# Performance work log

Measured on AMD Instinct MI355X. Metric: run time of the kernel, lower is better.

The kernel has to match this reference:

```python
import jax, jax.numpy as jnp
import numpy as np

T, B, S, D = 512, 32, 512, 512
EPS = 1e-6  # LayerNorm eps


def _ln(x, g, b):
    m = jnp.mean(x, axis=-1, keepdims=True)
    v = jnp.mean((x - m) ** 2, axis=-1, keepdims=True)
    return g * (x - m) * jax.lax.rsqrt(v + EPS) + b


def setup_inputs() -> dict:
    key = jax.random.key(0)
    ks = jax.random.split(key, 10)
    sc = 1.0 / np.sqrt(D).astype(np.float32)
    return {
        "prev_layer": jax.random.normal(ks[0], (T, B, D), jnp.float32),
        "hidden": jax.random.normal(ks[1], (B, D), jnp.float32),
        "enc_output": jax.random.normal(ks[2], (B, S, D), jnp.float32),
        "memory_length": jax.random.randint(ks[3], (B,), 1, S + 1),
        # nn.Linear weights stored as [in, out] (transposed torch layout)
        "W_in": jax.random.normal(ks[4], (D, 3 * D), jnp.float32) * sc,
        "W_enc": jax.random.normal(ks[5], (D, D), jnp.float32) * sc,
        "W_attn_in": jax.random.normal(ks[6], (D, D), jnp.float32) * sc,
        "W_hidden": jax.random.normal(ks[7], (D, D), jnp.float32) * sc,
        "W_ctx": jax.random.normal(ks[8], (D, D), jnp.float32) * sc,
        # LayerNorm gains/biases (5 LNs)
        "g_pre": jnp.ones((3 * D,), jnp.float32), "b_pre": jnp.zeros((3 * D,), jnp.float32),
        "g_enc": jnp.ones((D,), jnp.float32), "b_enc": jnp.zeros((D,), jnp.float32),
        "g_attn": jnp.ones((D,), jnp.float32), "b_attn": jnp.zeros((D,), jnp.float32),
        "g_h": jnp.ones((D,), jnp.float32), "b_h": jnp.zeros((D,), jnp.float32),
        "g_c": jnp.ones((D,), jnp.float32), "b_c": jnp.zeros((D,), jnp.float32),
    }


def reference(prev_layer, hidden, enc_output, W_in, W_enc, W_attn_in, W_hidden,
              W_ctx, g_pre, b_pre, g_enc, b_enc, g_attn, b_attn, g_h, b_h,
              g_c, b_c, memory_length):
    d = prev_layer.shape[-1]
    sqrt_d = jnp.sqrt(jnp.asarray(d, prev_layer.dtype))
    # dropout is identity in eval mode
    preact = _ln(prev_layer @ W_in, g_pre, b_pre)          # [T,B,3D]
    pctx = _ln(enc_output @ W_enc, g_enc, b_enc)           # [B,S,D]
    z, h_gate, pl_t = jnp.split(preact, 3, axis=-1)
    z = jax.nn.sigmoid(z)
    h_gate = jax.nn.sigmoid(h_gate)

    # SRU-style linear recurrence: s_t = (1-z_t)*s_{t-1} + z_t*pl_t
    def step(h, zp):
        z_t, p_t = zp
        s = (1.0 - z_t) * h + z_t * p_t
        return s, s

    hidden_last, ss = jax.lax.scan(step, hidden, (z, pl_t))  # ss: [T,B,D]

    attn_in = _ln(ss @ W_attn_in, g_attn, b_attn)            # [T,B,D]
    align = jnp.einsum('tbd,bsd->bts', attn_in, pctx)        # [B,T,S]
    mask = jnp.arange(pctx.shape[1])[None, :] < memory_length[:, None]  # [B,S]
    align = jnp.where(mask[:, None, :], align, -jnp.inf)
    av = jax.nn.softmax(align / sqrt_d, axis=-1)             # [B,T,S]
    c = jnp.einsum('bts,bsd->tbd', av, pctx)                 # [T,B,D]
    attn_out = c / sqrt_d

    trans = _ln(ss @ W_hidden, g_h, b_h) + _ln(attn_out @ W_ctx, g_c, b_c)
    out = jnp.tanh(trans)
    out = (1.0 - h_gate) * out + h_gate * prev_layer         # [T,B,D]
    p_attn = jnp.transpose(av, (1, 0, 2))                    # [T,B,S]
    return out, hidden_last, p_attn
```

## Files before the change

### kernel.cpp

```cpp
#include <hip/hip_runtime.h>
#include <hip/hip_bf16.h>
#include <cmath>

#define T_ 512
#define B_ 32
#define S_ 512
#define D_ 512
#define D3_ 1536
#define NCH 16
#define CT (T_ / NCH)
static constexpr float LN_EPS = 1e-6f;
static constexpr float RSQRT_D = 0.044194173824159216f;

typedef __attribute__((ext_vector_type(8))) __bf16 bf16x8;
typedef __attribute__((ext_vector_type(4))) float f32x4;

struct __align__(4) bfx2 { __hip_bfloat16 x, y; };
struct __align__(8) bfx4 { __hip_bfloat16 x, y, z, w; };

__device__ __forceinline__ void g2l16(const void* g, void* l) {
    __builtin_amdgcn_global_load_lds(
        (const __attribute__((address_space(1))) unsigned int*)g,
        (__attribute__((address_space(3))) unsigned int*)l, 16, 0, 0);
}

__device__ __forceinline__ float blk_sum(float v, float* sm) {
    v += __shfl_down(v, 32); v += __shfl_down(v, 16); v += __shfl_down(v, 8);
    v += __shfl_down(v, 4);  v += __shfl_down(v, 2);  v += __shfl_down(v, 1);
    int w = threadIdx.x >> 6;
    if ((threadIdx.x & 63) == 0) sm[w] = v;
    __syncthreads();
    float r = sm[0] + sm[1] + sm[2] + sm[3];
    __syncthreads();
    return r;
}

__device__ __forceinline__ float blk_max(float v, float* sm) {
    v = fmaxf(v, __shfl_down(v, 32)); v = fmaxf(v, __shfl_down(v, 16));
    v = fmaxf(v, __shfl_down(v, 8));  v = fmaxf(v, __shfl_down(v, 4));
    v = fmaxf(v, __shfl_down(v, 2));  v = fmaxf(v, __shfl_down(v, 1));
    int w = threadIdx.x >> 6;
    if ((threadIdx.x & 63) == 0) sm[w] = v;
    __syncthreads();
    float r = fmaxf(fmaxf(sm[0], sm[1]), fmaxf(sm[2], sm[3]));
    __syncthreads();
    return r;
}

template <typename OT>
__global__ __launch_bounds__(256) void gemm_bt(
    const __hip_bfloat16* __restrict__ A, int lda, long Abs,
    const __hip_bfloat16* __restrict__ B, int ldb, long Bbs,
    OT* __restrict__ C, long ldc, long Cbs,
    int K, float alpha)
{
    __shared__ __align__(16) __hip_bfloat16 As[128 * 32];
    __shared__ __align__(16) __hip_bfloat16 Bs[128 * 32];

    const int bz = blockIdx.z;
    A += (long)bz * Abs; B += (long)bz * Bbs; C += (long)bz * Cbs;
    const long bm = (long)blockIdx.y * 128, bn = (long)blockIdx.x * 128;

    const int tid = threadIdx.x, lane = tid & 63, w = tid >> 6;
    const int wm = (w >> 1) * 64, wn = (w & 1) * 64;
    const int srow = lane >> 2;
    const int skB = (lane & 3) * 16;

    f32x4 acc[4][4];
#pragma unroll
    for (int i = 0; i < 4; i++)
#pragma unroll
        for (int j = 0; j < 4; j++) acc[i][j] = (f32x4)(0.0f);

    const char* ga0 = (const char*)(A + (bm + w * 16 + srow) * (long)lda) + skB;
    const char* ga1 = (const char*)(A + (bm + (w + 4) * 16 + srow) * (long)lda) + skB;
    const char* gb0 = (const char*)(B + (bn + w * 16 + srow) * (long)ldb) + skB;
    const char* gb1 = (const char*)(B + (bn + (w + 4) * 16 + srow) * (long)ldb) + skB;
    char* la0 = (char*)As + w * 1024 + lane * 16;
    char* la1 = (char*)As + (w + 4) * 1024 + lane * 16;
    char* lb0 = (char*)Bs + w * 1024 + lane * 16;
    char* lb1 = (char*)Bs + (w + 4) * 1024 + lane * 16;

    const char* Ar = (const char*)As + (wm + (lane & 15)) * 64 + (lane >> 4) * 16;
    const char* Br = (const char*)Bs + (wn + (lane & 15)) * 64 + (lane >> 4) * 16;

    for (int k0 = 0; k0 < K; k0 += 32) {
        const long kb = (long)k0 * 2;
        g2l16(ga0 + kb, la0);
        g2l16(ga1 + kb, la1);
        g2l16(gb0 + kb, lb0);
        g2l16(gb1 + kb, lb1);
        __syncthreads();

        bf16x8 af[4], bfr[4];
#pragma unroll
        for (int i = 0; i < 4; i++) {
            af[i] = *(const bf16x8*)(Ar + i * 1024);
            bfr[i] = *(const bf16x8*)(Br + i * 1024);
        }
#pragma unroll
        for (int i = 0; i < 4; i++)
#pragma unroll
            for (int j = 0; j < 4; j++)
                acc[i][j] = __builtin_amdgcn_mfma_f32_16x16x32_bf16(
                    af[i], bfr[j], acc[i][j], 0, 0, 0);
        __syncthreads();
    }

#pragma unroll
    for (int i = 0; i < 4; i++) {
        const long row0 = bm + wm + i * 16 + (lane >> 4) * 4;
#pragma unroll
        for (int j = 0; j < 4; j++) {
            const long col = bn + wn + j * 16 + (lane & 15);
#pragma unroll
            for (int r = 0; r < 4; r++)
                C[(row0 + r) * ldc + col] = (OT)(alpha * acc[i][j][r]);
        }
    }
}

__global__ __launch_bounds__(256) void cvt4(
    const float* __restrict__ x, __hip_bfloat16* __restrict__ y, int n4)
{
    int i = blockIdx.x * 256 + threadIdx.x;
    if (i >= n4) return;
    float4 v = ((const float4*)x)[i];
    bfx4 o;
    o.x = __float2bfloat16(v.x); o.y = __float2bfloat16(v.y);
    o.z = __float2bfloat16(v.z); o.w = __float2bfloat16(v.w);
    ((bfx4*)y)[i] = o;
}

__global__ __launch_bounds__(256) void wtrans(
    const float* __restrict__ w0, const float* __restrict__ w1,
    const float* __restrict__ w2, const float* __restrict__ w3,
    const float* __restrict__ w4, __hip_bfloat16* __restrict__ WT)
{
    int z = blockIdx.z;
    const float* W; long off; int N;
    if (z == 0)      { W = w0; off = 0;                N = 1536; }
    else if (z == 1) { W = w1; off = 786432;           N = 512; }
    else if (z == 2) { W = w2; off = 786432 + 262144;  N = 512; }
    else if (z == 3) { W = w3; off = 786432 + 524288;  N = 512; }
    else             { W = w4; off = 786432 + 786432;  N = 512; }
    int n0 = blockIdx.x * 32, k0 = blockIdx.y * 32;
    if (n0 >= N) return;
    __shared__ float t[32][33];
    int tx = threadIdx.x & 31, ty = threadIdx.x >> 5;
#pragma unroll
    for (int i = 0; i < 4; i++)
        t[ty + i * 8][tx] = W[(long)(k0 + ty + i * 8) * N + n0 + tx];
    __syncthreads();
    __hip_bfloat16* O = WT + off;
#pragma unroll
    for (int i = 0; i < 4; i++)
        O[(long)(n0 + ty + i * 8) * 512 + k0 + tx] =
            __float2bfloat16(t[tx][ty + i * 8]);
}

__global__ __launch_bounds__(256) void ptrans(
    const __hip_bfloat16* __restrict__ src, __hip_bfloat16* __restrict__ dst)
{
    long boff = (long)blockIdx.z * (S_ * D_);
    int d0 = blockIdx.x * 32, s0 = blockIdx.y * 32;
    __shared__ __hip_bfloat16 t[32][34];
    int tx = threadIdx.x & 31, ty = threadIdx.x >> 5;
#pragma unroll
    for (int i = 0; i < 4; i++)
        t[ty + i * 8][tx] = src[boff + (long)(s0 + ty + i * 8) * D_ + d0 + tx];
    __syncthreads();
#pragma unroll
    for (int i = 0; i < 4; i++)
        dst[boff + (long)(d0 + ty + i * 8) * S_ + s0 + tx] = t[tx][ty + i * 8];
}

__global__ __launch_bounds__(256) void ln_rows(
    float* X, const float* __restrict__ g,
    const float* __restrict__ bb, int ncols, int sig_upto)
{
    __shared__ float sm[4];
    float* x = X + (long)blockIdx.x * ncols;
    float s = 0.f, q = 0.f;
    for (int c = threadIdx.x; c < ncols; c += 256) {
        float v = x[c]; s += v; q += v * v;
    }
    s = blk_sum(s, sm);
    q = blk_sum(q, sm);
    float m = s / ncols;
    float rs = rsqrtf(q / ncols - m * m + LN_EPS);
    for (int c = threadIdx.x; c < ncols; c += 256) {
        float v = (x[c] - m) * rs * g[c] + bb[c];
        if (c < sig_upto) v = 1.f / (1.f + __expf(-v));
        x[c] = v;
    }
}

__global__ __launch_bounds__(256) void ln_bf16(
    const float* __restrict__ X, const float* __restrict__ g,
    const float* __restrict__ bb, __hip_bfloat16* __restrict__ Y)
{
    __shared__ float sm[4];
    const float* x = X + (long)blockIdx.x * 512;
    int c = threadIdx.x * 2;
    float2 v = *(const float2*)(x + c);
    float s = v.x + v.y, q = v.x * v.x + v.y * v.y;
    s = blk_sum(s, sm);
    q = blk_sum(q, sm);
    float m = s * (1.f / 512);
    float rs = rsqrtf(q * (1.f / 512) - m * m + LN_EPS);
    float2 gg = *(const float2*)(g + c);
    float2 bv = *(const float2*)(bb + c);
    bfx2 o;
    o.x = __float2bfloat16((v.x - m) * rs * gg.x + bv.x);
    o.y = __float2bfloat16((v.y - m) * rs * gg.y + bv.y);
    *(bfx2*)(Y + (long)blockIdx.x * 512 + c) = o;
}

__global__ __launch_bounds__(256) void scan_part1(
    const float* __restrict__ pre, float* __restrict__ Ap, float* __restrict__ Bp)
{
    int idx = blockIdx.x * 256 + threadIdx.x;
    int c = blockIdx.y;
    const float* pz = pre + (long)(idx >> 9) * D3_ + (idx & 511);
    float A = 1.f, s = 0.f;
    for (int t = c * CT; t < (c + 1) * CT; t++) {
        const float* p = pz + (long)t * (B_ * D3_);
        float z = p[0], pl = p[2 * D_];
        float a = 1.f - z;
        A *= a;
        s = a * s + z * pl;
    }
    Ap[c * 16384 + idx] = A;
    Bp[c * 16384 + idx] = s;
}

__global__ __launch_bounds__(256) void scan_part2(
    const float* __restrict__ Ap, const float* __restrict__ Bp,
    const float* __restrict__ h0, float* __restrict__ sin_,
    float* __restrict__ hlast)
{
    int idx = blockIdx.x * 256 + threadIdx.x;
    float s = h0[idx];
    for (int c = 0; c < NCH; c++) {
        sin_[c * 16384 + idx] = s;
        s = Ap[c * 16384 + idx] * s + Bp[c * 16384 + idx];
    }
    hlast[idx] = s;
}

__global__ __launch_bounds__(256) void scan_part3(
    const float* __restrict__ pre, const float* __restrict__ sin_,
    __hip_bfloat16* __restrict__ ssb)
{
    int idx = blockIdx.x * 256 + threadIdx.x;
    int c = blockIdx.y;
    float s = sin_[c * 16384 + idx];
    const float* pz = pre + (long)(idx >> 9) * D3_ + (idx & 511);
    for (int t = c * CT; t < (c + 1) * CT; t++) {
        const float* p = pz + (long)t * (B_ * D3_);
        float z = p[0], pl = p[2 * D_];
        s += z * (pl - s);
        ssb[(long)t * 16384 + idx] = __float2bfloat16(s);
    }
}

__global__ __launch_bounds__(256) void softmax_mask(
    const float* __restrict__ align, const int* __restrict__ mlen,
    float* __restrict__ pattn, __hip_bfloat16* __restrict__ pattnb)
{
    __shared__ float sm[4];
    int b = blockIdx.x >> 9;
    int t = blockIdx.x & 511;
    const float* arow = align + ((long)b * T_ + t) * S_;
    long orow = ((long)t * B_ + b) * S_;
    int len = mlen[b];

    float mx = -INFINITY;
#pragma unroll
    for (int i = 0; i < 2; i++) {
        int s = threadIdx.x + i * 256;
        float v = (s < len) ? arow[s] : -INFINITY;
        mx = fmaxf(mx, v);
    }
    mx = blk_max(mx, sm);

    float e[2];
    float sum = 0.f;
#pragma unroll
    for (int i = 0; i < 2; i++) {
        int s = threadIdx.x + i * 256;
        float v = (s < len) ? __expf(arow[s] - mx) : 0.f;
        e[i] = v; sum += v;
    }
    sum = blk_sum(sum, sm);
    float inv = 1.f / sum;
#pragma unroll
    for (int i = 0; i < 2; i++) {
        int s = threadIdx.x + i * 256;
        float v = e[i] * inv;
        pattn[orow + s] = v;
        pattnb[orow + s] = __float2bfloat16(v);
    }
}

__global__ __launch_bounds__(256) void final_fuse(
    const float* __restrict__ h1, const float* __restrict__ h2,
    const float* __restrict__ pre, const float* __restrict__ prev,
    const float* __restrict__ g_h, const float* __restrict__ b_h,
    const float* __restrict__ g_c, const float* __restrict__ b_c,
    float* __restrict__ out)
{
    __shared__ float sm[4];
    long row = blockIdx.x;
    const float* x1 = h1 + row * D_;
    const float* x2 = h2 + row * D_;
    float v1[2], v2[2];
    float s1 = 0, q1 = 0, s2 = 0, q2 = 0;
#pragma unroll
    for (int i = 0; i < 2; i++) {
        int c = threadIdx.x + i * 256;
        float a = x1[c], b = x2[c];
        v1[i] = a; v2[i] = b;
        s1 += a; q1 += a * a; s2 += b; q2 += b * b;
    }
    s1 = blk_sum(s1, sm); q1 = blk_sum(q1, sm);
    s2 = blk_sum(s2, sm); q2 = blk_sum(q2, sm);
    float m1 = s1 / D_, m2 = s2 / D_;
    float rs1 = rsqrtf(q1 / D_ - m1 * m1 + LN_EPS);
    float rs2 = rsqrtf(q2 / D_ - m2 * m2 + LN_EPS);
#pragma unroll
    for (int i = 0; i < 2; i++) {
        int c = threadIdx.x + i * 256;
        float t1 = (v1[i] - m1) * rs1 * g_h[c] + b_h[c];
        float t2 = (v2[i] - m2) * rs2 * g_c[c] + b_c[c];
        float o = tanhf(t1 + t2);
        float hg = pre[row * D3_ + D_ + c];
        float pv = prev[row * D_ + c];
        out[row * D_ + c] = (1.f - hg) * o + hg * pv;
    }
}

extern "C" void kernel_launch(void* const* d_in, const int* in_sizes, int n_in,
                              void* d_out, int out_size, void* d_ws, size_t ws_size,
                              hipStream_t stream) {
    const float* prev  = (const float*)d_in[0];
    const float* hid0  = (const float*)d_in[1];
    const float* enc   = (const float*)d_in[2];
    const int*   mlen  = (const int*)  d_in[3];
    const float* W_in  = (const float*)d_in[4];
    const float* W_enc = (const float*)d_in[5];
    const float* W_att = (const float*)d_in[6];
    const float* W_hid = (const float*)d_in[7];
    const float* W_ctx = (const float*)d_in[8];
    const float* g_pre = (const float*)d_in[9];
    const float* b_pre = (const float*)d_in[10];
    const float* g_enc = (const float*)d_in[11];
    const float* b_enc = (const float*)d_in[12];
    const float* g_att = (const float*)d_in[13];
    const float* b_att = (const float*)d_in[14];
    const float* g_h   = (const float*)d_in[15];
    const float* b_h   = (const float*)d_in[16];
    const float* g_c   = (const float*)d_in[17];
    const float* b_c   = (const float*)d_in[18];

    float* out   = (float*)d_out;
    float* hlast = out + (long)T_ * B_ * D_;
    float* pattn = hlast + (long)B_ * D_;

    float* ws = (float*)d_ws;
    const long MBf = 262144;
    float* pre              = ws;
    __hip_bfloat16* WT      = (__hip_bfloat16*)(ws + 96 * MBf);
    __hip_bfloat16* prevb   = (__hip_bfloat16*)(ws + 100 * MBf);
    __hip_bfloat16* encb    = (__hip_bfloat16*)(ws + 116 * MBf);
    float* pctxf            = ws + 132 * MBf;
    __hip_bfloat16* pctxb   = (__hip_bfloat16*)(ws + 164 * MBf);
    __hip_bfloat16* pctxT   = (__hip_bfloat16*)(ws + 180 * MBf);
    __hip_bfloat16* ssb     = (__hip_bfloat16*)(ws + 196 * MBf);
    float* scanA            = ws + 212 * MBf;
    float* scanB            = ws + 213 * MBf;
    float* sinb             = ws + 214 * MBf;
    float* attninf          = ws + 100 * MBf;
    __hip_bfloat16* attninb = (__hip_bfloat16*)(ws + 132 * MBf);
    float* algn             = ws + 212 * MBf;
    __hip_bfloat16* pattnb  = (__hip_bfloat16*)(ws + 148 * MBf);
    __hip_bfloat16* attnoutb= (__hip_bfloat16*)(ws + 100 * MBf);
    float* h1f              = ws + 116 * MBf;
    float* h2f              = ws + 148 * MBf;

    const long R = (long)T_ * B_;
    const __hip_bfloat16* W_inT  = WT;
    const __hip_bfloat16* W_encT = WT + 786432;
    const __hip_bfloat16* W_attT = WT + 786432 + 262144;
    const __hip_bfloat16* W_hidT = WT + 786432 + 524288;
    const __hip_bfloat16* W_ctxT = WT + 786432 + 786432;

    dim3 blk(256);

    cvt4<<<8192, blk, 0, stream>>>(prev, prevb, (int)(R * D_ / 4));
    cvt4<<<8192, blk, 0, stream>>>(enc, encb, (int)(R * D_ / 4));
    wtrans<<<dim3(48, 16, 5), blk, 0, stream>>>(W_in, W_enc, W_att, W_hid, W_ctx,
                                                (__hip_bfloat16*)WT);

    gemm_bt<float><<<dim3(12, 128, 1), blk, 0, stream>>>(
        prevb, D_, 0, W_inT, D_, 0, pre, D3_, 0, D_, 1.f);
    ln_rows<<<R, blk, 0, stream>>>(pre, g_pre, b_pre, D3_, 2 * D_);

    gemm_bt<float><<<dim3(4, 128, 1), blk, 0, stream>>>(
        encb, D_, 0, W_encT, D_, 0, pctxf, D_, 0, D_, 1.f);
    ln_bf16<<<R, blk, 0, stream>>>(pctxf, g_enc, b_enc, pctxb);
    ptrans<<<dim3(16, 16, 32), blk, 0, stream>>>(pctxb, pctxT);

    scan_part1<<<dim3(64, NCH), blk, 0, stream>>>(pre, scanA, scanB);
    scan_part2<<<64, blk, 0, stream>>>(scanA, scanB, hid0, sinb, hlast);
    scan_part3<<<dim3(64, NCH), blk, 0, stream>>>(pre, sinb, ssb);

    gemm_bt<float><<<dim3(4, 128, 1), blk, 0, stream>>>(
        ssb, D_, 0, W_attT, D_, 0, attninf, D_, 0, D_, 1.f);
    ln_bf16<<<R, blk, 0, stream>>>(attninf, g_att, b_att, attninb);

    gemm_bt<float><<<dim3(4, 4, 32), blk, 0, stream>>>(
        attninb, B_ * D_, D_, pctxb, D_, (long)S_ * D_,
        algn, S_, (long)T_ * S_, D_, RSQRT_D);

    softmax_mask<<<B_ * T_, blk, 0, stream>>>(algn, mlen, pattn, pattnb);

    gemm_bt<__hip_bfloat16><<<dim3(4, 4, 32), blk, 0, stream>>>(
        pattnb, B_ * S_, S_, pctxT, S_, (long)D_ * S_,
        attnoutb, B_ * D_, D_, S_, RSQRT_D);

    gemm_bt<float><<<dim3(4, 128, 1), blk, 0, stream>>>(
        ssb, D_, 0, W_hidT, D_, 0, h1f, D_, 0, D_, 1.f);
    gemm_bt<float><<<dim3(4, 128, 1), blk, 0, stream>>>(
        attnoutb, D_, 0, W_ctxT, D_, 0, h2f, D_, 0, D_, 1.f);

    final_fuse<<<R, blk, 0, stream>>>(h1f, h2f, pre, prev,
                                      g_h, b_h, g_c, b_c, out);
}
```

Before: 504.8 us.

## Fuse LayerNorm, softmax and gating epilogues into full-row GEMM kernels

Replaces the generic GEMM plus separate LayerNorm, softmax and final-gating kernels with specialized GEMMs. Each block computes full 512-wide rows so row statistics, the masked softmax and the tanh/gate epilogue can be applied in registers. The input projection now writes bf16 output plus per-row partial sums, and the pre-activation LayerNorm is applied on the fly inside the scan and final kernels. This removes several fp32 intermediate round trips through HBM and many launches. In exchange the new kernels use more registers and shared memory, and 64-row tiles give fewer blocks (256 per GEMM), which may lower occupancy.

After: 574.0 us. +13.7%, slower.

```diff
diff --git a/kernel.cpp b/kernel.cpp
--- a/kernel.cpp
+++ b/kernel.cpp
@@ -15,7 +15,6 @@
 typedef __attribute__((ext_vector_type(8))) __bf16 bf16x8;
 typedef __attribute__((ext_vector_type(4))) float f32x4;
 
-struct __align__(4) bfx2 { __hip_bfloat16 x, y; };
 struct __align__(8) bfx4 { __hip_bfloat16 x, y, z, w; };
 
 __device__ __forceinline__ void g2l16(const void* g, void* l) {
@@ -24,47 +23,34 @@
         (__attribute__((address_space(3))) unsigned int*)l, 16, 0, 0);
 }
 
-__device__ __forceinline__ float blk_sum(float v, float* sm) {
-    v += __shfl_down(v, 32); v += __shfl_down(v, 16); v += __shfl_down(v, 8);
-    v += __shfl_down(v, 4);  v += __shfl_down(v, 2);  v += __shfl_down(v, 1);
-    int w = threadIdx.x >> 6;
-    if ((threadIdx.x & 63) == 0) sm[w] = v;
-    __syncthreads();
-    float r = sm[0] + sm[1] + sm[2] + sm[3];
-    __syncthreads();
-    return r;
-}
-
-__device__ __forceinline__ float blk_max(float v, float* sm) {
-    v = fmaxf(v, __shfl_down(v, 32)); v = fmaxf(v, __shfl_down(v, 16));
-    v = fmaxf(v, __shfl_down(v, 8));  v = fmaxf(v, __shfl_down(v, 4));
-    v = fmaxf(v, __shfl_down(v, 2));  v = fmaxf(v, __shfl_down(v, 1));
-    int w = threadIdx.x >> 6;
-    if ((threadIdx.x & 63) == 0) sm[w] = v;
-    __syncthreads();
-    float r = fmaxf(fmaxf(sm[0], sm[1]), fmaxf(sm[2], sm[3]));
-    __syncthreads();
-    return r;
-}
-
-template <typename OT>
-__global__ __launch_bounds__(256) void gemm_bt(
-    const __hip_bfloat16* __restrict__ A, int lda, long Abs,
-    const __hip_bfloat16* __restrict__ B, int ldb, long Bbs,
-    OT* __restrict__ C, long ldc, long Cbs,
-    int K, float alpha)
-{
-    __shared__ __align__(16) __hip_bfloat16 As[128 * 32];
-    __shared__ __align__(16) __hip_bfloat16 Bs[128 * 32];
-
-    const int bz = blockIdx.z;
-    A += (long)bz * Abs; B += (long)bz * Bbs; C += (long)bz * Cbs;
-    const long bm = (long)blockIdx.y * 128, bn = (long)blockIdx.x * 128;
-
+__device__ __forceinline__ float xr_sum16(float v) {
+    v += __shfl_xor(v, 1); v += __shfl_xor(v, 2);
+    v += __shfl_xor(v, 4); v += __shfl_xor(v, 8); return v;
+}
+__device__ __forceinline__ float xr_max16(float v) {
+    v = fmaxf(v, __shfl_xor(v, 1)); v = fmaxf(v, __shfl_xor(v, 2));
+    v = fmaxf(v, __shfl_xor(v, 4)); v = fmaxf(v, __shfl_xor(v, 8)); return v;
+}
+
+__device__ __forceinline__ float sigmoidf_(float x) {
+    return 1.f / (1.f + __expf(-x));
+}
+
+__global__ __launch_bounds__(256) void gemm_pre(
+    const __hip_bfloat16* __restrict__ A,
+    const __hip_bfloat16* __restrict__ Bw,
+    __hip_bfloat16* __restrict__ preb,
+    float2* __restrict__ part)
+{
+    __shared__ char smem[16384];
+    __hip_bfloat16* As = (__hip_bfloat16*)smem;
+    __hip_bfloat16* Bs = (__hip_bfloat16*)(smem + 8192);
+
+    const int m0 = blockIdx.y * 128, n0 = blockIdx.x * 128;
     const int tid = threadIdx.x, lane = tid & 63, w = tid >> 6;
     const int wm = (w >> 1) * 64, wn = (w & 1) * 64;
-    const int srow = lane >> 2;
-    const int skB = (lane & 3) * 16;
+    const int srow = lane >> 2, skB = (lane & 3) * 16;
+    const int q = lane >> 4, c = lane & 15;
 
     f32x4 acc[4][4];
 #pragma unroll
@@ -72,26 +58,24 @@
 #pragma unroll
         for (int j = 0; j < 4; j++) acc[i][j] = (f32x4)(0.0f);
 
-    const char* ga0 = (const char*)(A + (bm + w * 16 + srow) * (long)lda) + skB;
-    const char* ga1 = (const char*)(A + (bm + (w + 4) * 16 + srow) * (long)lda) + skB;
-    const char* gb0 = (const char*)(B + (bn + w * 16 + srow) * (long)ldb) + skB;
-    const char* gb1 = (const char*)(B + (bn + (w + 4) * 16 + srow) * (long)ldb) + skB;
+    const char* ga0 = (const char*)(A + (long)(m0 + w * 16 + srow) * 512) + skB;
+    const char* ga1 = (const char*)(A + (long)(m0 + (w + 4) * 16 + srow) * 512) + skB;
+    const char* gb0 = (const char*)(Bw + (long)(n0 + w * 16 + srow) * 512) + skB;
+    const char* gb1 = (const char*)(Bw + (long)(n0 + (w + 4) * 16 + srow) * 512) + skB;
     char* la0 = (char*)As + w * 1024 + lane * 16;
     char* la1 = (char*)As + (w + 4) * 1024 + lane * 16;
     char* lb0 = (char*)Bs + w * 1024 + lane * 16;
     char* lb1 = (char*)Bs + (w + 4) * 1024 + lane * 16;
-
-    const char* Ar = (const char*)As + (wm + (lane & 15)) * 64 + (lane >> 4) * 16;
-    const char* Br = (const char*)Bs + (wn + (lane & 15)) * 64 + (lane >> 4) * 16;
-
-    for (int k0 = 0; k0 < K; k0 += 32) {
+    const char* Ar = (const char*)As + (wm + c) * 64 + q * 16;
+    const char* Br = (const char*)Bs + (wn + c) * 64 + q * 16;
+
+    for (int k0 = 0; k0 < 512; k0 += 32) {
         const long kb = (long)k0 * 2;
         g2l16(ga0 + kb, la0);
         g2l16(ga1 + kb, la1);
         g2l16(gb0 + kb, lb0);
         g2l16(gb1 + kb, lb1);
         __syncthreads();
-
         bf16x8 af[4], bfr[4];
 #pragma unroll
         for (int i = 0; i < 4; i++) {
@@ -107,15 +91,374 @@
         __syncthreads();
     }
 
-#pragma unroll
-    for (int i = 0; i < 4; i++) {
-        const long row0 = bm + wm + i * 16 + (lane >> 4) * 4;
-#pragma unroll
-        for (int j = 0; j < 4; j++) {
-            const long col = bn + wn + j * 16 + (lane & 15);
-#pragma unroll
-            for (int r = 0; r < 4; r++)
-                C[(row0 + r) * ldc + col] = (OT)(alpha * acc[i][j][r]);
+    float2* sred = (float2*)smem;
+#pragma unroll
+    for (int i = 0; i < 4; i++)
+#pragma unroll
+        for (int r = 0; r < 4; r++) {
+            float s = 0.f, qq = 0.f;
+#pragma unroll
+            for (int j = 0; j < 4; j++) {
+                float v = acc[i][j][r]; s += v; qq += v * v;
+            }
+            s = xr_sum16(s); qq = xr_sum16(qq);
+            if (c == 0) sred[(wm + i * 16 + q * 4 + r) * 2 + (w & 1)] =
+                make_float2(s, qq);
+        }
+    __syncthreads();
+    if ((w & 1) == 0 && c == 0) {
+#pragma unroll
+        for (int i = 0; i < 4; i++)
+#pragma unroll
+            for (int r = 0; r < 4; r++) {
+                int row = wm + i * 16 + q * 4 + r;
+                float2 a = sred[row * 2], b2 = sred[row * 2 + 1];
+                part[(long)blockIdx.x * 16384 + m0 + row] =
+                    make_float2(a.x + b2.x, a.y + b2.y);
+            }
+    }
+    __syncthreads();
+
+    for (int p = 0; p < 2; p++) {
+        if ((w >> 1) == p) {
+#pragma unroll
+            for (int i = 0; i < 4; i++)
+#pragma unroll
+                for (int j = 0; j < 4; j++)
+#pragma unroll
+                    for (int r = 0; r < 4; r++) {
+                        int row = i * 16 + q * 4 + r;
+                        int col = wn + j * 16 + c;
+                        ((__hip_bfloat16*)smem)[row * 128 + col] =
+                            __float2bfloat16(acc[i][j][r]);
+                    }
+        }
+        __syncthreads();
+#pragma unroll
+        for (int rnd = 0; rnd < 4; rnd++) {
+            int row = rnd * 16 + (tid >> 4);
+            int ch = tid & 15;
+            uint4 v = *(const uint4*)(smem + row * 256 + ch * 16);
+            long grow = m0 + p * 64 + row;
+            *(uint4*)((char*)preb + grow * 3072 + (long)n0 * 2 + ch * 16) = v;
+        }
+        __syncthreads();
+    }
+}
+
+__device__ __forceinline__ void rows_core(
+    const __hip_bfloat16* A, long lda,
+    const __hip_bfloat16* B, long ldb, int K,
+    char* smem, f32x4 (&acc)[4][8])
+{
+    const int tid = threadIdx.x, lane = tid & 63, w = tid >> 6;
+#pragma unroll
+    for (int m = 0; m < 4; m++)
+#pragma unroll
+        for (int j = 0; j < 8; j++) acc[m][j] = (f32x4)(0.0f);
+
+    const char* ga = (const char*)(A + (long)(w * 16 + (lane >> 2)) * lda) + (lane & 3) * 16;
+    char* la = smem + w * 1024 + lane * 16;
+    const char* gb = (const char*)(B + (long)(w * 128 + (lane >> 2)) * ldb) + (lane & 3) * 16;
+    char* lb = smem + 4096 + w * 8192 + lane * 16;
+    const long ldbB16 = (long)ldb * 32;
+    const char* Ar = smem + (lane & 15) * 64 + (lane >> 4) * 16;
+    const char* Br = smem + 4096 + (w * 128 + (lane & 15)) * 64 + (lane >> 4) * 16;
+
+    for (int k0 = 0; k0 < K; k0 += 32) {
+        const long kb = (long)k0 * 2;
+        g2l16(ga + kb, la);
+#pragma unroll
+        for (int s = 0; s < 8; s++) g2l16(gb + kb + s * ldbB16, lb + s * 1024);
+        __syncthreads();
+        bf16x8 af[4], bfr[8];
+#pragma unroll
+        for (int m = 0; m < 4; m++) af[m] = *(const bf16x8*)(Ar + m * 1024);
+#pragma unroll
+        for (int j = 0; j < 8; j++) bfr[j] = *(const bf16x8*)(Br + j * 1024);
+#pragma unroll
+        for (int m = 0; m < 4; m++)
+#pragma unroll
+            for (int j = 0; j < 8; j++)
+                acc[m][j] = __builtin_amdgcn_mfma_f32_16x16x32_bf16(
+                    af[m], bfr[j], acc[m][j], 0, 0, 0);
+        __syncthreads();
+    }
+}
+
+__global__ __launch_bounds__(256, 2) void gemm_ln(
+    const __hip_bfloat16* __restrict__ A, long lda,
+    const __hip_bfloat16* __restrict__ W,
+    const float* __restrict__ g, const float* __restrict__ bb,
+    __hip_bfloat16* __restrict__ out)
+{
+    __shared__ char smem[36864];
+    const long m0 = (long)blockIdx.y * 64;
+    f32x4 acc[4][8];
+    rows_core(A + m0 * lda, lda, W, 512, 512, smem, acc);
+
+    const int tid = threadIdx.x, lane = tid & 63, w = tid >> 6;
+    const int q = lane >> 4, c = lane & 15;
+    float2* sred = (float2*)smem;
+    float mean[4][4], rstd[4][4];
+#pragma unroll
+    for (int m = 0; m < 4; m++)
+#pragma unroll
+        for (int r = 0; r < 4; r++) {
+            float s = 0.f, qq = 0.f;
+#pragma unroll
+            for (int j = 0; j < 8; j++) {
+                float v = acc[m][j][r]; s += v; qq += v * v;
+            }
+            s = xr_sum16(s); qq = xr_sum16(qq);
+            if (c == 0) sred[(m * 16 + q * 4 + r) * 4 + w] = make_float2(s, qq);
+        }
+    __syncthreads();
+#pragma unroll
+    for (int m = 0; m < 4; m++)
+#pragma unroll
+        for (int r = 0; r < 4; r++) {
+            int row = m * 16 + q * 4 + r;
+            float s = 0.f, qq = 0.f;
+#pragma unroll
+            for (int ww = 0; ww < 4; ww++) {
+                float2 t = sred[row * 4 + ww]; s += t.x; qq += t.y;
+            }
+            float mn = s * (1.f / 512);
+            mean[m][r] = mn;
+            rstd[m][r] = rsqrtf(qq * (1.f / 512) - mn * mn + LN_EPS);
+        }
+    __syncthreads();
+    float gv[8], bv[8];
+#pragma unroll
+    for (int j = 0; j < 8; j++) {
+        int col = w * 128 + j * 16 + c;
+        gv[j] = g[col]; bv[j] = bb[col];
+    }
+    for (int m = 0; m < 4; m++) {
+#pragma unroll
+        for (int j = 0; j < 8; j++)
+#pragma unroll
+            for (int r = 0; r < 4; r++) {
+                int row = q * 4 + r;
+                int col = w * 128 + j * 16 + c;
+                float v = (acc[m][j][r] - mean[m][r]) * rstd[m][r] * gv[j] + bv[j];
+                ((__hip_bfloat16*)smem)[row * 512 + col] = __float2bfloat16(v);
+            }
+        __syncthreads();
+#pragma unroll
+        for (int rnd = 0; rnd < 4; rnd++) {
+            int row = rnd * 4 + w;
+            uint4 v = *(const uint4*)(smem + row * 1024 + lane * 16);
+            *(uint4*)((char*)out + (m0 + m * 16 + row) * 1024 + lane * 16) = v;
+        }
+        __syncthreads();
+    }
+}
+
+__global__ __launch_bounds__(256, 2) void gemm_attn(
+    const __hip_bfloat16* __restrict__ attninb,
+    const __hip_bfloat16* __restrict__ pctxb,
+    const int* __restrict__ mlen,
+    float* __restrict__ pattn, __hip_bfloat16* __restrict__ pattnb)
+{
+    __shared__ char smem[36864];
+    const int b = blockIdx.z;
+    const long t0 = (long)blockIdx.y * 64;
+    f32x4 acc[4][8];
+    rows_core(attninb + (long)b * 512 + t0 * 16384, 16384,
+              pctxb + (long)b * 262144, 512, 512, smem, acc);
+
+    const int tid = threadIdx.x, lane = tid & 63, w = tid >> 6;
+    const int q = lane >> 4, c = lane & 15;
+    const int len = mlen[b];
+    float* sred = (float*)smem;
+
+    float rmax[4][4];
+#pragma unroll
+    for (int m = 0; m < 4; m++)
+#pragma unroll
+        for (int r = 0; r < 4; r++) {
+            float mx = -INFINITY;
+#pragma unroll
+            for (int j = 0; j < 8; j++) {
+                int col = w * 128 + j * 16 + c;
+                float v = acc[m][j][r] * RSQRT_D;
+                acc[m][j][r] = v;
+                if (col < len) mx = fmaxf(mx, v);
+            }
+            mx = xr_max16(mx);
+            if (c == 0) sred[(m * 16 + q * 4 + r) * 4 + w] = mx;
+        }
+    __syncthreads();
+#pragma unroll
+    for (int m = 0; m < 4; m++)
+#pragma unroll
+        for (int r = 0; r < 4; r++) {
+            int row = m * 16 + q * 4 + r;
+            rmax[m][r] = fmaxf(fmaxf(sred[row * 4], sred[row * 4 + 1]),
+                               fmaxf(sred[row * 4 + 2], sred[row * 4 + 3]));
+        }
+    __syncthreads();
+    float rinv[4][4];
+#pragma unroll
+    for (int m = 0; m < 4; m++)
+#pragma unroll
+        for (int r = 0; r < 4; r++) {
+            float s = 0.f;
+#pragma unroll
+            for (int j = 0; j < 8; j++) {
+                int col = w * 128 + j * 16 + c;
+                float e = (col < len) ? __expf(acc[m][j][r] - rmax[m][r]) : 0.f;
+                acc[m][j][r] = e; s += e;
+            }
+            s = xr_sum16(s);
+            if (c == 0) sred[(m * 16 + q * 4 + r) * 4 + w] = s;
+        }
+    __syncthreads();
+#pragma unroll
+    for (int m = 0; m < 4; m++)
+#pragma unroll
+        for (int r = 0; r < 4; r++) {
+            int row = m * 16 + q * 4 + r;
+            float s = sred[row * 4] + sred[row * 4 + 1] +
+                      sred[row * 4 + 2] + sred[row * 4 + 3];
+            rinv[m][r] = 1.f / s;
+        }
+    __syncthreads();
+
+#pragma unroll
+    for (int m = 0; m < 4; m++)
+#pragma unroll
+        for (int j = 0; j < 8; j++)
+#pragma unroll
+            for (int r = 0; r < 4; r++) {
+                int row = m * 16 + q * 4 + r;
+                int col = w * 128 + j * 16 + c;
+                float p = acc[m][j][r] * rinv[m][r];
+                acc[m][j][r] = p;
+                pattn[((t0 + row) * 32 + b) * 512 + col] = p;
+            }
+    for (int m = 0; m < 4; m++) {
+#pragma unroll
+        for (int j = 0; j < 8; j++)
+#pragma unroll
+            for (int r = 0; r < 4; r++) {
+                int row = q * 4 + r;
+                int col = w * 128 + j * 16 + c;
+                ((__hip_bfloat16*)smem)[row * 512 + col] =
+                    __float2bfloat16(acc[m][j][r]);
+            }
+        __syncthreads();
+#pragma unroll
+        for (int rnd = 0; rnd < 4; rnd++) {
+            int row = rnd * 4 + w;
+            uint4 v = *(const uint4*)(smem + row * 1024 + lane * 16);
+            *(uint4*)((char*)pattnb + ((t0 + m * 16 + row) * 32 + b) * 1024 +
+                      lane * 16) = v;
+        }
+        __syncthreads();
+    }
+}
+
+__global__ __launch_bounds__(256, 2) void gemm_av(
+    const __hip_bfloat16* __restrict__ pattnb,
+    const __hip_bfloat16* __restrict__ pctxT,
+    __hip_bfloat16* __restrict__ attnoutb)
+{
+    __shared__ char smem[36864];
+    const int b = blockIdx.z;
+    const long t0 = (long)blockIdx.y * 64;
+    f32x4 acc[4][8];
+    rows_core(pattnb + (long)b * 512 + t0 * 16384, 16384,
+              pctxT + (long)b * 262144, 512, 512, smem, acc);
+
+    const int tid = threadIdx.x, lane = tid & 63, w = tid >> 6;
+    const int q = lane >> 4, c = lane & 15;
+    for (int m = 0; m < 4; m++) {
+#pragma unroll
+        for (int j = 0; j < 8; j++)
+#pragma unroll
+            for (int r = 0; r < 4; r++) {
+                int row = q * 4 + r;
+                int col = w * 128 + j * 16 + c;
+                ((__hip_bfloat16*)smem)[row * 512 + col] =
+                    __float2bfloat16(acc[m][j][r] * RSQRT_D);
+            }
+        __syncthreads();
+#pragma unroll
+        for (int rnd = 0; rnd < 4; rnd++) {
+            int row = rnd * 4 + w;
+            uint4 v = *(const uint4*)(smem + row * 1024 + lane * 16);
+            *(uint4*)((char*)attnoutb + ((t0 + m * 16 + row) * 32 + b) * 1024 +
+                      lane * 16) = v;
+        }
+        __syncthreads();
+    }
+}
+
+__global__ __launch_bounds__(256, 2) void gemm_fin(
+    const __hip_bfloat16* __restrict__ attnoutb,
+    const __hip_bfloat16* __restrict__ Wc,
+    const __hip_bfloat16* __restrict__ h1n,
+    const __hip_bfloat16* __restrict__ preb,
+    const float2* __restrict__ stats,
+    const float* __restrict__ g_c, const float* __restrict__ b_c,
+    const float* __restrict__ g_pre, const float* __restrict__ b_pre,
+    const float* __restrict__ prev, float* __restrict__ out)
+{
+    __shared__ char smem[36864];
+    const long m0 = (long)blockIdx.y * 64;
+    f32x4 acc[4][8];
+    rows_core(attnoutb + m0 * 512, 512, Wc, 512, 512, smem, acc);
+
+    const int tid = threadIdx.x, lane = tid & 63, w = tid >> 6;
+    const int q = lane >> 4, c = lane & 15;
+    float2* sred = (float2*)smem;
+#pragma unroll
+    for (int m = 0; m < 4; m++)
+#pragma unroll
+        for (int r = 0; r < 4; r++) {
+            float s = 0.f, qq = 0.f;
+#pragma unroll
+            for (int j = 0; j < 8; j++) {
+                float v = acc[m][j][r]; s += v; qq += v * v;
+            }
+            s = xr_sum16(s); qq = xr_sum16(qq);
+            if (c == 0) sred[(m * 16 + q * 4 + r) * 4 + w] = make_float2(s, qq);
+        }
+    __syncthreads();
+    float gcv[8], bcv[8], gpv[8], bpv[8];
+#pragma unroll
+    for (int j = 0; j < 8; j++) {
+        int col = w * 128 + j * 16 + c;
+        gcv[j] = g_c[col]; bcv[j] = b_c[col];
+        gpv[j] = g_pre[512 + col]; bpv[j] = b_pre[512 + col];
+    }
+    for (int m = 0; m < 4; m++) {
+#pragma unroll
+        for (int r = 0; r < 4; r++) {
+            int row = m * 16 + q * 4 + r;
+            float s = 0.f, qq = 0.f;
+#pragma unroll
+            for (int ww = 0; ww < 4; ww++) {
+                float2 t = sred[row * 4 + ww]; s += t.x; qq += t.y;
+            }
+            float mn = s * (1.f / 512);
+            float rs = rsqrtf(qq * (1.f / 512) - mn * mn + LN_EPS);
+            long rowg = m0 + row;
+            float2 sh = stats[rowg];
+#pragma unroll
+            for (int j = 0; j < 8; j++) {
+                int col = w * 128 + j * 16 + c;
+                float t2 = (acc[m][j][r] - mn) * rs * gcv[j] + bcv[j];
+                float t1 = __bfloat162float(h1n[rowg * 512 + col]);
+                float hraw = __bfloat162float(preb[rowg * 1536 + 512 + col]);
+                float hg = sigmoidf_((hraw - sh.x) * sh.y * gpv[j] + bpv[j]);
+                float pv = prev[rowg * 512 + col];
+                float o = tanhf(t1 + t2);
+                out[rowg * 512 + col] = (1.f - hg) * o + hg * pv;
+            }
         }
     }
 }
@@ -175,64 +518,44 @@
         dst[boff + (long)(d0 + ty + i * 8) * S_ + s0 + tx] = t[tx][ty + i * 8];
 }
 
-__global__ __launch_bounds__(256) void ln_rows(
-    float* X, const float* __restrict__ g,
-    const float* __restrict__ bb, int ncols, int sig_upto)
-{
-    __shared__ float sm[4];
-    float* x = X + (long)blockIdx.x * ncols;
-    float s = 0.f, q = 0.f;
-    for (int c = threadIdx.x; c < ncols; c += 256) {
-        float v = x[c]; s += v; q += v * v;
-    }
-    s = blk_sum(s, sm);
-    q = blk_sum(q, sm);
-    float m = s / ncols;
-    float rs = rsqrtf(q / ncols - m * m + LN_EPS);
-    for (int c = threadIdx.x; c < ncols; c += 256) {
-        float v = (x[c] - m) * rs * g[c] + bb[c];
-        if (c < sig_upto) v = 1.f / (1.f + __expf(-v));
-        x[c] = v;
-    }
-}
-
-__global__ __launch_bounds__(256) void ln_bf16(
-    const float* __restrict__ X, const float* __restrict__ g,
-    const float* __restrict__ bb, __hip_bfloat16* __restrict__ Y)
-{
-    __shared__ float sm[4];
-    const float* x = X + (long)blockIdx.x * 512;
-    int c = threadIdx.x * 2;
-    float2 v = *(const float2*)(x + c);
-    float s = v.x + v.y, q = v.x * v.x + v.y * v.y;
-    s = blk_sum(s, sm);
-    q = blk_sum(q, sm);
-    float m = s * (1.f / 512);
-    float rs = rsqrtf(q * (1.f / 512) - m * m + LN_EPS);
-    float2 gg = *(const float2*)(g + c);
-    float2 bv = *(const float2*)(bb + c);
-    bfx2 o;
-    o.x = __float2bfloat16((v.x - m) * rs * gg.x + bv.x);
-    o.y = __float2bfloat16((v.y - m) * rs * gg.y + bv.y);
-    *(bfx2*)(Y + (long)blockIdx.x * 512 + c) = o;
+__global__ __launch_bounds__(256) void stats_fin(
+    const float2* __restrict__ part, float2* __restrict__ stats)
+{
+    int r = blockIdx.x * 256 + threadIdx.x;
+    float s = 0.f, qq = 0.f;
+#pragma unroll
+    for (int cb = 0; cb < 12; cb++) {
+        float2 v = part[(long)cb * 16384 + r]; s += v.x; qq += v.y;
+    }
+    float m = s * (1.f / 1536);
+    float rs = rsqrtf(qq * (1.f / 1536) - m * m + LN_EPS);
+    stats[r] = make_float2(m, rs);
 }
 
 __global__ __launch_bounds__(256) void scan_part1(
-    const float* __restrict__ pre, float* __restrict__ Ap, float* __restrict__ Bp)
+    const __hip_bfloat16* __restrict__ preb, const float2* __restrict__ stats,
+    const float* __restrict__ gpre, const float* __restrict__ bpre,
+    float* __restrict__ Ap, float* __restrict__ Bp)
 {
     int idx = blockIdx.x * 256 + threadIdx.x;
-    int c = blockIdx.y;
-    const float* pz = pre + (long)(idx >> 9) * D3_ + (idx & 511);
+    int b = idx >> 9, d = idx & 511;
+    int ch = blockIdx.y;
+    float gz = gpre[d], bz = bpre[d];
+    float gp = gpre[1024 + d], bpv = bpre[1024 + d];
     float A = 1.f, s = 0.f;
-    for (int t = c * CT; t < (c + 1) * CT; t++) {
-        const float* p = pz + (long)t * (B_ * D3_);
-        float z = p[0], pl = p[2 * D_];
+    for (int t = ch * CT; t < (ch + 1) * CT; t++) {
+        long row = (long)t * 32 + b;
+        float2 st = stats[row];
+        float zr = __bfloat162float(preb[row * 1536 + d]);
+        float pr = __bfloat162float(preb[row * 1536 + 1024 + d]);
+        float z = sigmoidf_((zr - st.x) * st.y * gz + bz);
+        float pl = (pr - st.x) * st.y * gp + bpv;
         float a = 1.f - z;
         A *= a;
         s = a * s + z * pl;
     }
-    Ap[c * 16384 + idx] = A;
-    Bp[c * 16384 + idx] = s;
+    Ap[ch * 16384 + idx] = A;
+    Bp[ch * 16384 + idx] = s;
 }
 
 __global__ __launch_bounds__(256) void scan_part2(
@@ -242,102 +565,33 @@
 {
     int idx = blockIdx.x * 256 + threadIdx.x;
     float s = h0[idx];
-    for (int c = 0; c < NCH; c++) {
-        sin_[c * 16384 + idx] = s;
-        s = Ap[c * 16384 + idx] * s + Bp[c * 16384 + idx];
+    for (int ch = 0; ch < NCH; ch++) {
+        sin_[ch * 16384 + idx] = s;
+        s = Ap[ch * 16384 + idx] * s + Bp[ch * 16384 + idx];
     }
     hlast[idx] = s;
 }
 
 __global__ __launch_bounds__(256) void scan_part3(
-    const float* __restrict__ pre, const float* __restrict__ sin_,
-    __hip_bfloat16* __restrict__ ssb)
+    const __hip_bfloat16* __restrict__ preb, const float2* __restrict__ stats,
+    const float* __restrict__ gpre, const float* __restrict__ bpre,
+    const float* __restrict__ sin_, __hip_bfloat16* __restrict__ ssb)
 {
     int idx = blockIdx.x * 256 + threadIdx.x;
-    int c = blockIdx.y;
-    float s = sin_[c * 16384 + idx];
-    const float* pz = pre + (long)(idx >> 9) * D3_ + (idx & 511);
-    for (int t = c * CT; t < (c + 1) * CT; t++) {
-        const float* p = pz + (long)t * (B_ * D3_);
-        float z = p[0], pl = p[2 * D_];
+    int b = idx >> 9, d = idx & 511;
+    int ch = blockIdx.y;
+    float gz = gpre[d], bz = bpre[d];
+    float gp = gpre[1024 + d], bpv = bpre[1024 + d];
+    float s = sin_[ch * 16384 + idx];
+    for (int t = ch * CT; t < (ch + 1) * CT; t++) {
+        long row = (long)t * 32 + b;
+        float2 st = stats[row];
+        float zr = __bfloat162float(preb[row * 1536 + d]);
+        float pr = __bfloat162float(preb[row * 1536 + 1024 + d]);
+        float z = sigmoidf_((zr - st.x) * st.y * gz + bz);
+        float pl = (pr - st.x) * st.y * gp + bpv;
         s += z * (pl - s);
         ssb[(long)t * 16384 + idx] = __float2bfloat16(s);
-    }
-}
-
-__global__ __launch_bounds__(256) void softmax_mask(
-    const float* __restrict__ align, const int* __restrict__ mlen,
-    float* __restrict__ pattn, __hip_bfloat16* __restrict__ pattnb)
-{
-    __shared__ float sm[4];
-    int b = blockIdx.x >> 9;
-    int t = blockIdx.x & 511;
-    const float* arow = align + ((long)b * T_ + t) * S_;
-    long orow = ((long)t * B_ + b) * S_;
-    int len = mlen[b];
-
-    float mx = -INFINITY;
-#pragma unroll
-    for (int i = 0; i < 2; i++) {
-        int s = threadIdx.x + i * 256;
-        float v = (s < len) ? arow[s] : -INFINITY;
-        mx = fmaxf(mx, v);
-    }
-    mx = blk_max(mx, sm);
-
-    float e[2];
-    float sum = 0.f;
-#pragma unroll
-    for (int i = 0; i < 2; i++) {
-        int s = threadIdx.x + i * 256;
-        float v = (s < len) ? __expf(arow[s] - mx) : 0.f;
-        e[i] = v; sum += v;
-    }
-    sum = blk_sum(sum, sm);
-    float inv = 1.f / sum;
-#pragma unroll
-    for (int i = 0; i < 2; i++) {
-        int s = threadIdx.x + i * 256;
-        float v = e[i] * inv;
-        pattn[orow + s] = v;
-        pattnb[orow + s] = __float2bfloat16(v);
-    }
-}
-
-__global__ __launch_bounds__(256) void final_fuse(
-    const float* __restrict__ h1, const float* __restrict__ h2,
-    const float* __restrict__ pre, const float* __restrict__ prev,
-    const float* __restrict__ g_h, const float* __restrict__ b_h,
-    const float* __restrict__ g_c, const float* __restrict__ b_c,
-    float* __restrict__ out)
-{
-    __shared__ float sm[4];
-    long row = blockIdx.x;
-    const float* x1 = h1 + row * D_;
-    const float* x2 = h2 + row * D_;
-    float v1[2], v2[2];
-    float s1 = 0, q1 = 0, s2 = 0, q2 = 0;
-#pragma unroll
-    for (int i = 0; i < 2; i++) {
-        int c = threadIdx.x + i * 256;
-        float a = x1[c], b = x2[c];
-        v1[i] = a; v2[i] = b;
-        s1 += a; q1 += a * a; s2 += b; q2 += b * b;
-    }
-    s1 = blk_sum(s1, sm); q1 = blk_sum(q1, sm);
-    s2 = blk_sum(s2, sm); q2 = blk_sum(q2, sm);
-    float m1 = s1 / D_, m2 = s2 / D_;
-    float rs1 = rsqrtf(q1 / D_ - m1 * m1 + LN_EPS);
-    float rs2 = rsqrtf(q2 / D_ - m2 * m2 + LN_EPS);
-#pragma unroll
-    for (int i = 0; i < 2; i++) {
-        int c = threadIdx.x + i * 256;
-        float t1 = (v1[i] - m1) * rs1 * g_h[c] + b_h[c];
-        float t2 = (v2[i] - m2) * rs2 * g_c[c] + b_c[c];
-        float o = tanhf(t1 + t2);
-        float hg = pre[row * D3_ + D_ + c];
-        float pv = prev[row * D_ + c];
-        out[row * D_ + c] = (1.f - hg) * o + hg * pv;
     }
 }
 
@@ -368,29 +622,24 @@
     float* hlast = out + (long)T_ * B_ * D_;
     float* pattn = hlast + (long)B_ * D_;
 
-    float* ws = (float*)d_ws;
-    const long MBf = 262144;
-    float* pre              = ws;
-    __hip_bfloat16* WT      = (__hip_bfloat16*)(ws + 96 * MBf);
-    __hip_bfloat16* prevb   = (__hip_bfloat16*)(ws + 100 * MBf);
-    __hip_bfloat16* encb    = (__hip_bfloat16*)(ws + 116 * MBf);
-    float* pctxf            = ws + 132 * MBf;
-    __hip_bfloat16* pctxb   = (__hip_bfloat16*)(ws + 164 * MBf);
-    __hip_bfloat16* pctxT   = (__hip_bfloat16*)(ws + 180 * MBf);
-    __hip_bfloat16* ssb     = (__hip_bfloat16*)(ws + 196 * MBf);
-    float* scanA            = ws + 212 * MBf;
-    float* scanB            = ws + 213 * MBf;
-    float* sinb             = ws + 214 * MBf;
-    float* attninf          = ws + 100 * MBf;
-    __hip_bfloat16* attninb = (__hip_bfloat16*)(ws + 132 * MBf);
-    float* algn             = ws + 212 * MBf;
-    __hip_bfloat16* pattnb  = (__hip_bfloat16*)(ws + 148 * MBf);
-    __hip_bfloat16* attnoutb= (__hip_bfloat16*)(ws + 100 * MBf);
-    float* h1f              = ws + 116 * MBf;
-    float* h2f              = ws + 148 * MBf;
-
-    const long R = (long)T_ * B_;
-    const __hip_bfloat16* W_inT  = WT;
+    char* ws = (char*)d_ws;
+    __hip_bfloat16* preb    = (__hip_bfloat16*)(ws);
+    __hip_bfloat16* WT      = (__hip_bfloat16*)(ws + 50331648);
+    __hip_bfloat16* prevb   = (__hip_bfloat16*)(ws + 54525952);
+    __hip_bfloat16* encb    = (__hip_bfloat16*)(ws + 71303168);
+    __hip_bfloat16* pctxb   = (__hip_bfloat16*)(ws + 88080384);
+    __hip_bfloat16* pctxT   = (__hip_bfloat16*)(ws + 104857600);
+    __hip_bfloat16* ssb     = (__hip_bfloat16*)(ws + 121634816);
+    __hip_bfloat16* attninb = (__hip_bfloat16*)(ws + 138412032);
+    __hip_bfloat16* pattnb  = (__hip_bfloat16*)(ws + 155189248);
+    __hip_bfloat16* attnoutb= (__hip_bfloat16*)(ws + 171966464);
+    __hip_bfloat16* h1n     = (__hip_bfloat16*)(ws + 188743680);
+    float2* part            = (float2*)(ws + 205520896);
+    float2* stats           = (float2*)(ws + 207093760);
+    float* scanA            = (float*)(ws + 207224832);
+    float* scanB            = (float*)(ws + 208273408);
+    float* sinb             = (float*)(ws + 209321984);
+
     const __hip_bfloat16* W_encT = WT + 786432;
     const __hip_bfloat16* W_attT = WT + 786432 + 262144;
     const __hip_bfloat16* W_hidT = WT + 786432 + 524288;
@@ -398,43 +647,35 @@
 
     dim3 blk(256);
 
-    cvt4<<<8192, blk, 0, stream>>>(prev, prevb, (int)(R * D_ / 4));
-    cvt4<<<8192, blk, 0, stream>>>(enc, encb, (int)(R * D_ / 4));
-    wtrans<<<dim3(48, 16, 5), blk, 0, stream>>>(W_in, W_enc, W_att, W_hid, W_ctx,
-                                                (__hip_bfloat16*)WT);
-
-    gemm_bt<float><<<dim3(12, 128, 1), blk, 0, stream>>>(
-        prevb, D_, 0, W_inT, D_, 0, pre, D3_, 0, D_, 1.f);
-    ln_rows<<<R, blk, 0, stream>>>(pre, g_pre, b_pre, D3_, 2 * D_);
-
-    gemm_bt<float><<<dim3(4, 128, 1), blk, 0, stream>>>(
-        encb, D_, 0, W_encT, D_, 0, pctxf, D_, 0, D_, 1.f);
-    ln_bf16<<<R, blk, 0, stream>>>(pctxf, g_enc, b_enc, pctxb);
+    cvt4<<<8192, blk, 0, stream>>>(prev, prevb, 2097152);
+    cvt4<<<8192, blk, 0, stream>>>(enc, encb, 2097152);
+    wtrans<<<dim3(48, 16, 5), blk, 0, stream>>>(W_in, W_enc, W_att, W_hid,
+                                                W_ctx, WT);
+
+    gemm_pre<<<dim3(12, 128), blk, 0, stream>>>(prevb, WT, preb, part);
+    stats_fin<<<64, blk, 0, stream>>>(part, stats);
+
+    scan_part1<<<dim3(64, NCH), blk, 0, stream>>>(preb, stats, g_pre, b_pre,
+                                                  scanA, scanB);
+    scan_part2<<<64, blk, 0, stream>>>(scanA, scanB, hid0, sinb, hlast);
+    scan_part3<<<dim3(64, NCH), blk, 0, stream>>>(preb, stats, g_pre, b_pre,
+                                                  sinb, ssb);
+
+    gemm_ln<<<dim3(1, 256), blk, 0, stream>>>(encb, 512, W_encT, g_enc, b_enc,
+                                              pctxb);
     ptrans<<<dim3(16, 16, 32), blk, 0, stream>>>(pctxb, pctxT);
 
-    scan_part1<<<dim3(64, NCH), blk, 0, stream>>>(pre, scanA, scanB);
-    scan_part2<<<64, blk, 0, stream>>>(scanA, scanB, hid0, sinb, hlast);
-    scan_part3<<<dim3(64, NCH), blk, 0, stream>>>(pre, sinb, ssb);
-
-    gemm_bt<float><<<dim3(4, 128, 1), blk, 0, stream>>>(
-        ssb, D_, 0, W_attT, D_, 0, attninf, D_, 0, D_, 1.f);
-    ln_bf16<<<R, blk, 0, stream>>>(attninf, g_att, b_att, attninb);
-
-    gemm_bt<float><<<dim3(4, 4, 32), blk, 0, stream>>>(
-        attninb, B_ * D_, D_, pctxb, D_, (long)S_ * D_,
-        algn, S_, (long)T_ * S_, D_, RSQRT_D);
-
-    softmax_mask<<<B_ * T_, blk, 0, stream>>>(algn, mlen, pattn, pattnb);
-
-    gemm_bt<__hip_bfloat16><<<dim3(4, 4, 32), blk, 0, stream>>>(
-        pattnb, B_ * S_, S_, pctxT, S_, (long)D_ * S_,
-        attnoutb, B_ * D_, D_, S_, RSQRT_D);
-
-    gemm_bt<float><<<dim3(4, 128, 1), blk, 0, stream>>>(
-        ssb, D_, 0, W_hidT, D_, 0, h1f, D_, 0, D_, 1.f);
-    gemm_bt<float><<<dim3(4, 128, 1), blk, 0, stream>>>(
-        attnoutb, D_, 0, W_ctxT, D_, 0, h2f, D_, 0, D_, 1.f);
-
-    final_fuse<<<R, blk, 0, stream>>>(h1f, h2f, pre, prev,
-                                      g_h, b_h, g_c, b_c, out);
-}
+    gemm_ln<<<dim3(1, 256), blk, 0, stream>>>(ssb, 512, W_attT, g_att, b_att,
+                                              attninb);
+
+    gemm_attn<<<dim3(1, 8, 32), blk, 0, stream>>>(attninb, pctxb, mlen,
+                                                  pattn, pattnb);
+
+    gemm_av<<<dim3(1, 8, 32), blk, 0, stream>>>(pattnb, pctxT, attnoutb);
+
+    gemm_ln<<<dim3(1, 256), blk, 0, stream>>>(ssb, 512, W_hidT, g_h, b_h, h1n);
+
+    gemm_fin<<<dim3(1, 256), blk, 0, stream>>>(attnoutb, W_ctxT, h1n, preb,
+                                               stats, g_c, b_c, g_pre, b_pre,
+                                               prev, out);
+}
```
